# Performance work log

Hardware: AMD Instinct MI355X
Metric: run time of the kernel (lower is better)

## Reference

```python
import jax, jax.numpy as jnp
import numpy as np

N = 100000   # nodes
E = 1600000  # edges
IN = 128
H = 64
OUT = 10
NG = 128     # number of graphs
EPS = 1e-5


def _lin(k, o, i):
    kw, kb = jax.random.split(k)
    bound = 1.0 / np.sqrt(i)
    W = jax.random.uniform(kw, (o, i), jnp.float32, -bound, bound)
    b = jax.random.uniform(kb, (o,), jnp.float32, -bound, bound)
    return W, b


def setup_inputs() -> dict:
    key = jax.random.key(0)
    ks = jax.random.split(key, 10)
    x = jax.random.normal(ks[0], (N, IN), jnp.float32)
    edge_index = jax.random.randint(ks[1], (2, E), 0, N, dtype=jnp.int64)
    batch = jnp.sort(jax.random.randint(ks[2], (N,), 0, NG, dtype=jnp.int64))
    W1, b1 = _lin(ks[3], H, IN)
    W2, b2 = _lin(ks[4], H, H)
    W3, b3 = _lin(ks[5], H, H)
    Wc1, bc1 = _lin(ks[6], H, H)
    Wc2, bc2 = _lin(ks[7], OUT, H)
    ones = jnp.ones((H,), jnp.float32)
    zeros = jnp.zeros((H,), jnp.float32)
    return {
        "x": x, "edge_index": edge_index, "batch": batch,
        "W1": W1, "b1": b1, "g1": ones, "be1": zeros,
        "W2": W2, "b2": b2, "g2": ones, "be2": zeros,
        "W3": W3, "b3": b3, "g3": ones, "be3": zeros,
        "Wc1": Wc1, "bc1": bc1, "Wc2": Wc2, "bc2": bc2,
    }


def reference(x, edge_index, batch,
              W1, b1, g1, be1, W2, b2, g2, be2, W3, b3, g3, be3,
              Wc1, bc1, Wc2, bc2):
    n = x.shape[0]
    src, dst = edge_index[0], edge_index[1]
    loop = jnp.arange(n, dtype=src.dtype)
    src_a = jnp.concatenate([src, loop])  # [E+N] with self loops
    dst_a = jnp.concatenate([dst, loop])
    # degree via scatter-add (self loops included -> deg >= 1)
    deg = jax.ops.segment_sum(jnp.ones_like(dst_a, jnp.float32), dst_a, num_segments=n)
    norm = (deg[src_a] * deg[dst_a]) ** -0.5
    norm = jnp.where(jnp.isinf(norm), 0.0, norm)  # guard deg==0 (faithful to source)

    def conv(h, W, b):
        h = h @ W.T + b                       # [N, H]
        msg = h[src_a] * norm[:, None]        # gather + scale  [E+N, H]
        return jax.ops.segment_sum(msg, dst_a, num_segments=n)  # scatter-add

    def bn_relu(h, g, be):
        mu = h.mean(0)
        var = h.var(0)  # biased variance (torch BN training mode)
        return jax.nn.relu(g * (h - mu) / jnp.sqrt(var + EPS) + be)

    for (W, b, g, be) in [(W1, b1, g1, be1), (W2, b2, g2, be2), (W3, b3, g3, be3)]:
        x = bn_relu(conv(x, W, b), g, be)

    pool = jax.ops.segment_sum(x, batch, num_segments=NG)  # readout='sum'
    h = jax.nn.relu(pool @ Wc1.T + bc1)
    return h @ Wc2.T + bc2
```

## Files before the change

### kernel.cpp

```cpp
#include <hip/hip_runtime.h>
#include <hip/hip_bf16.h>


#define NN 100000
#define NE 1600000
#define INF_ 128
#define HF 64
#define OUTF 10
#define NG 128
#define NBUCK 196
#define NBLKP 512
#define CPB (NE / NBLKP)
#define NPART 32

typedef short bf16x8 __attribute__((ext_vector_type(8)));
typedef float f32x4 __attribute__((ext_vector_type(4)));

static __device__ __forceinline__ unsigned short f2bf(float x) {
    unsigned int b = __float_as_uint(x);
    b += 0x7FFFu + ((b >> 16) & 1u);
    return (unsigned short)(b >> 16);
}
static __device__ __forceinline__ float bf2f(unsigned short u) {
    return __uint_as_float(((unsigned int)u) << 16);
}
static __device__ __forceinline__ float bflo(unsigned int u) {
    return __uint_as_float(u << 16);
}
static __device__ __forceinline__ float bfhi(unsigned int u) {
    return __uint_as_float(u & 0xffff0000u);
}

__global__ __launch_bounds__(256) void kA_count(const int* __restrict__ dst,
                                                int* __restrict__ gcount) {
    __shared__ int cnt[256];
    int t = threadIdx.x, blk = blockIdx.x;
    cnt[t] = 0;
    __syncthreads();
    int beg = blk * CPB, end = beg + CPB;
    for (int i = beg + t; i < end; i += 256) atomicAdd(&cnt[dst[i] >> 9], 1);
    __syncthreads();
    if (t < NBUCK) gcount[t * NBLKP + blk] = cnt[t];
}

__global__ void k_scan1(const int* __restrict__ cnt, int* __restrict__ ro,
                        int* __restrict__ bsum, int n) {
    __shared__ int ts[256];
    int base = blockIdx.x * 1024 + threadIdx.x * 4;
    int v[4], s = 0;
#pragma unroll
    for (int k = 0; k < 4; ++k) {
        int idx = base + k;
        v[k] = (idx < n) ? cnt[idx] : 0;
        s += v[k];
    }
    ts[threadIdx.x] = s;
    __syncthreads();
    for (int off = 1; off < 256; off <<= 1) {
        int t = (threadIdx.x >= off) ? ts[threadIdx.x - off] : 0;
        __syncthreads();
        ts[threadIdx.x] += t;
        __syncthreads();
    }
    int ex = ts[threadIdx.x] - s;
    if (threadIdx.x == 255) bsum[blockIdx.x] = ts[255];
#pragma unroll
    for (int k = 0; k < 4; ++k) {
        int idx = base + k;
        if (idx < n) ro[idx] = ex;
        ex += v[k];
    }
}

__global__ void k_scan2(int* __restrict__ bsum, int nb) {
    __shared__ int ts[128];
    int i = threadIdx.x;
    int v = (i < nb) ? bsum[i] : 0;
    ts[i] = v;
    __syncthreads();
    for (int off = 1; off < 128; off <<= 1) {
        int t = (i >= off) ? ts[i - off] : 0;
        __syncthreads();
        ts[i] += t;
        __syncthreads();
    }
    if (i < nb) bsum[i] = ts[i] - v;
}

__global__ void k_scan3g(int* __restrict__ goff, const int* __restrict__ bsum, int n) {
    int i = blockIdx.x * 256 + threadIdx.x;
    if (i < n) goff[i] += bsum[i >> 10];
}

__global__ __launch_bounds__(256) void kB_part(const int* __restrict__ src,
                                               const int* __restrict__ dst,
                                               const int* __restrict__ goff,
                                               int* __restrict__ tmp) {
    __shared__ int cur[NBUCK];
    int t = threadIdx.x, blk = blockIdx.x;
    if (t < NBUCK) cur[t] = goff[t * NBLKP + blk];
    __syncthreads();
    int beg = blk * CPB, end = beg + CPB;
    for (int i = beg + t; i < end; i += 256) {
        int d = dst[i];
        int pos = atomicAdd(&cur[d >> 9], 1);
        tmp[pos] = ((d & 511) << 17) | src[i];
    }
}

__global__ __launch_bounds__(256) void kC_build(const int* __restrict__ goff,
                                                int* __restrict__ tmp,
                                                int* __restrict__ ss,
                                                int* __restrict__ ro,
                                                float* __restrict__ rdeg, int E) {
    __shared__ int cnt[512];
    __shared__ int ts[256];
    __shared__ int cur[512];
    int t = threadIdx.x, b = blockIdx.x;
    int beg = goff[b * NBLKP];
    int end = (b + 1 < NBUCK) ? goff[(b + 1) * NBLKP] : E;
    cnt[t] = 0;
    cnt[t + 256] = 0;
    __syncthreads();
    for (int i = beg + t; i < end; i += 256) atomicAdd(&cnt[tmp[i] >> 17], 1);
    __syncthreads();
    int a0 = cnt[2 * t], a1 = cnt[2 * t + 1], s = a0 + a1;
    ts[t] = s;
    __syncthreads();
    for (int off = 1; off < 256; off <<= 1) {
        int v = (t >= off) ? ts[t - off] : 0;
        __syncthreads();
        ts[t] += v;
        __syncthreads();
    }
    int ex = ts[t] - s;
    int p0 = beg + ex, p1 = beg + ex + a0;
    cur[2 * t] = p0;
    cur[2 * t + 1] = p1;
    int node0 = (b << 9) + 2 * t;
    if (node0 < NN) { ro[node0] = p0; rdeg[node0] = rsqrtf((float)a0 + 1.f); }
    else if (node0 == NN) ro[NN] = p0;
    int node1 = node0 + 1;
    if (node1 < NN) { ro[node1] = p1; rdeg[node1] = rsqrtf((float)a1 + 1.f); }
    else if (node1 == NN) ro[NN] = p1;
    __syncthreads();
    for (int i = beg + t; i < end; i += 256) {
        int p = tmp[i];
        int pos = atomicAdd(&cur[p >> 17], 1);
        ss[pos] = p & 0x1FFFF;
    }
}

__global__ void k_wpack_all(const float* __restrict__ W1f, const float* __restrict__ W2f,
                            const float* __restrict__ W3f,
                            unsigned short* __restrict__ wp0,
                            unsigned short* __restrict__ wp1,
                            unsigned short* __restrict__ wp2) {
    int b = blockIdx.x;
    const float* W;
    unsigned short* P;
    int K, base;
    if (b < 4)      { W = W1f; P = wp0; K = INF_; base = b; }
    else if (b < 6) { W = W2f; P = wp1; K = HF;   base = b - 4; }
    else            { W = W3f; P = wp2; K = HF;   base = b - 6; }
    int q = base * 256 + threadIdx.x;
    int nchunk = (K >> 5) << 8;
    if (q >= nchunk) return;
    int kb = q >> 8;
    int gq = (q >> 6) & 3;
    int ch = q & 63;
    const float* wr = W + (size_t)ch * K;
    unsigned int u[4];
#pragma unroll
    for (int i = 0; i < 4; ++i) {
        int e0 = 2 * i, e1 = 2 * i + 1;
        int k0 = kb * 32 + 4 * gq + (e0 & 3) + 16 * (e0 >> 2);
        int k1 = kb * 32 + 4 * gq + (e1 & 3) + 16 * (e1 >> 2);
        u[i] = (unsigned int)f2bf(wr[k0]) | ((unsigned int)f2bf(wr[k1]) << 16);
    }
    *(uint4*)(P + (size_t)q * 8) = make_uint4(u[0], u[1], u[2], u[3]);
}

template<int K, bool BN>
__global__ __launch_bounds__(256) void k_gemm_mfma(const float* __restrict__ Xf,
                                                   const unsigned short* __restrict__ Xh,
                                                   const unsigned short* __restrict__ Wp,
                                                   const float* __restrict__ bias,
                                                   const float* __restrict__ rdeg,
                                                   const float* __restrict__ SP,
                                                   const float* __restrict__ g,
                                                   const float* __restrict__ be,
                                                   unsigned short* __restrict__ Hs, int n) {
    constexpr int KB = K / 32;
    constexpr int RB = K * 2;
    __shared__ __align__(16) char raw[64 * 68 * 4];
    __shared__ float sa_l[64], sb_l[64];
    const int t = threadIdx.x;
    const int w = t >> 6;
    const int c = t & 15;
    const int gq = (t >> 4) & 3;
    const int r0 = blockIdx.x * 64;

    if (BN && t < 64) {
        float s = 0.f, q = 0.f;
#pragma unroll
        for (int p = 0; p < NPART; ++p) {
            s += SP[p * 128 + t];
            q += SP[p * 128 + 64 + t];
        }
        float n_ = (float)NN;
        float mu = s / n_;
        float var = q / n_ - mu * mu;
        float a = g[t] * rsqrtf(var + 1e-5f);
        sa_l[t] = a;
        sb_l[t] = be[t] - mu * a;
    }
    __syncthreads();

    {
        int r = t >> 2, q = t & 3;
        int row = r0 + r;
        int x_swz = (r & 7) << 4;
        if (BN) {
            int ch0 = q * 16;
            uint4 u0 = make_uint4(0, 0, 0, 0), u1 = make_uint4(0, 0, 0, 0);
            if (row < n) {
                const uint4* p = (const uint4*)(Xh + (size_t)row * 64 + ch0);
                u0 = p[0];
                u1 = p[1];
            }
            unsigned int uin[8] = {u0.x, u0.y, u0.z, u0.w, u1.x, u1.y, u1.z, u1.w};
            unsigned int uo[8];
#pragma unroll
            for (int j = 0; j < 8; ++j) {
                int chl = ch0 + 2 * j, chh = chl + 1;
                float v0 = fmaxf(fmaf(sa_l[chl], bflo(uin[j]), sb_l[chl]), 0.f);
                float v1 = fmaxf(fmaf(sa_l[chh], bfhi(uin[j]), sb_l[chh]), 0.f);
                uo[j] = (unsigned int)f2bf(v0) | ((unsigned int)f2bf(v1) << 16);
            }
            int b0 = r * RB + q * 32;
            *(uint4*)(raw + ((b0) ^ x_swz)) = make_uint4(uo[0], uo[1], uo[2], uo[3]);
            *(uint4*)(raw + ((b0 + 16) ^ x_swz)) = make_uint4(uo[4], uo[5], uo[6], uo[7]);
        } else {
            int ch0 = q * 32;
#pragma unroll
            for (int j2 = 0; j2 < 4; ++j2) {
                float4 a = make_float4(0.f, 0.f, 0.f, 0.f), b = make_float4(0.f, 0.f, 0.f, 0.f);
                if (row < n) {
                    const float4* p = (const float4*)(Xf + (size_t)row * K + ch0 + j2 * 8);
                    a = p[0];
                    b = p[1];
                }
                unsigned int q0 = (unsigned int)f2bf(a.x) | ((unsigned int)f2bf(a.y) << 16);
                unsigned int q1 = (unsigned int)f2bf(a.z) | ((unsigned int)f2bf(a.w) << 16);
                unsigned int q2 = (unsigned int)f2bf(b.x) | ((unsigned int)f2bf(b.y) << 16);
                unsigned int q3 = (unsigned int)f2bf(b.z) | ((unsigned int)f2bf(b.w) << 16);
                int b0 = r * RB + ch0 * 2 + j2 * 16;
                *(uint4*)(raw + (b0 ^ x_swz)) = make_uint4(q0, q1, q2, q3);
            }
        }
    }
    __syncthreads();

    bf16x8 af[KB];
    {
        int r = 16 * w + c;
        int rb = r * RB;
        int swz = (r & 7) << 4;
#pragma unroll
        for (int kb = 0; kb < KB; ++kb) {
            int off = rb + kb * 64 + gq * 8;
            uint2 u0 = *(const uint2*)(raw + (off ^ swz));
            uint2 u1 = *(const uint2*)(raw + ((off + 32) ^ swz));
            union { uint4 u; bf16x8 v; } cv;
            cv.u = make_uint4(u0.x, u0.y, u1.x, u1.y);
            af[kb] = cv.v;
        }
    }
    const uint4* wq = (const uint4*)Wp;
    f32x4 acc[4];
#pragma unroll
    for (int nn_ = 0; nn_ < 4; ++nn_) {
        acc[nn_] = (f32x4){0.f, 0.f, 0.f, 0.f};
#pragma unroll
        for (int kb = 0; kb < KB; ++kb) {
            union { uint4 u; bf16x8 v; } cw;
            cw.u = wq[(kb * 4 + gq) * 64 + nn_ * 16 + c];
            acc[nn_] = __builtin_amdgcn_mfma_f32_16x16x32_bf16(af[kb], cw.v, acc[nn_], 0, 0, 0);
        }
    }

    __syncthreads();
    float* outb = (float*)raw;
    float rv[4];
#pragma unroll
    for (int i = 0; i < 4; ++i) {
        int rg = r0 + 16 * w + 4 * gq + i;
        rv[i] = (rg < n) ? rdeg[rg] : 0.f;
    }
#pragma unroll
    for (int nn_ = 0; nn_ < 4; ++nn_) {
        int col = 16 * nn_ + c;
        float bz = bias[col];
#pragma unroll
        for (int i = 0; i < 4; ++i)
            outb[(16 * w + 4 * gq + i) * 68 + col] = (acc[nn_][i] + bz) * rv[i];
    }
    __syncthreads();
    {
        int r = t >> 2, q = t & 3;
        int row = r0 + r;
        if (row < n) {
            const float* src = outb + r * 68 + q * 16;
            unsigned int u[8];
#pragma unroll
            for (int j = 0; j < 8; ++j)
                u[j] = (unsigned int)f2bf(src[2 * j]) | ((unsigned int)f2bf(src[2 * j + 1]) << 16);
            uint4* p = (uint4*)(Hs + (size_t)row * HF + q * 16);
            p[0] = make_uint4(u[0], u[1], u[2], u[3]);
            p[1] = make_uint4(u[4], u[5], u[6], u[7]);
        }
    }
}

__global__ __launch_bounds__(256) void k_agg(const int* __restrict__ ro,
                                             const int* __restrict__ ss,
                                             const unsigned short* __restrict__ Hs,
                                             const float* __restrict__ rdeg,
                                             unsigned short* __restrict__ V16,
                                             float* __restrict__ partial, int n) {
    __shared__ float red[4][128];
    int t = threadIdx.x;
    int wid = blockIdx.x * 4 + (t >> 6);
    int lane = t & 63;
    int sub = lane >> 4;
    int lq = lane & 15;
    int c4 = lq * 4;
    int node = wid * 4 + sub;
    bool vn = node < n;
    int safe = vn ? node : 0;
    int beg = 0, d = 0;
    if (vn) {
        beg = ro[node];
        d = ro[node + 1] - beg;
    }
    float4 acc = make_float4(0.f, 0.f, 0.f, 0.f);
    if (vn) {
        uint2 u = *(const uint2*)(Hs + ((size_t)node << 6) + c4);
        acc.x = bflo(u.x); acc.y = bfhi(u.x); acc.z = bflo(u.y); acc.w = bfhi(u.y);
    }
    int dm = d;
    dm = max(dm, __shfl_xor(dm, 16));
    dm = max(dm, __shfl_xor(dm, 32));
    for (int it = 0; it < dm; it += 16) {
        int myidx = (it + lq < d) ? ss[beg + it + lq] : -1;
        int sidx[16];
        float msk[16];
#pragma unroll
        for (int k = 0; k < 16; ++k) {
            int s = __shfl(myidx, (sub << 4) + k);
            sidx[k] = (s >= 0) ? s : safe;
            msk[k] = (s >= 0) ? 1.f : 0.f;
        }
        uint2 u[16];
#pragma unroll
        for (int k = 0; k < 16; ++k)
            u[k] = *(const uint2*)(Hs + ((size_t)sidx[k] << 6) + c4);
#pragma unroll
        for (int k = 0; k < 16; ++k) {
            acc.x = fmaf(msk[k], bflo(u[k].x), acc.x);
            acc.y = fmaf(msk[k], bfhi(u[k].x), acc.y);
            acc.z = fmaf(msk[k], bflo(u[k].y), acc.z);
            acc.w = fmaf(msk[k], bfhi(u[k].y), acc.w);
        }
    }
    float rv = vn ? rdeg[node] : 0.f;
    float v0 = acc.x * rv, v1 = acc.y * rv, v2 = acc.z * rv, v3 = acc.w * rv;
    if (vn) {
        unsigned int p0 = (unsigned int)f2bf(v0) | ((unsigned int)f2bf(v1) << 16);
        unsigned int p1 = (unsigned int)f2bf(v2) | ((unsigned int)f2bf(v3) << 16);
        *(uint2*)(V16 + ((size_t)node << 6) + c4) = make_uint2(p0, p1);
    }
    float s0 = v0, s1 = v1, s2 = v2, s3 = v3;
    float q0 = v0 * v0, q1 = v1 * v1, q2 = v2 * v2, q3 = v3 * v3;
#pragma unroll
    for (int m = 16; m <= 32; m <<= 1) {
        s0 += __shfl_xor(s0, m); s1 += __shfl_xor(s1, m);
        s2 += __shfl_xor(s2, m); s3 += __shfl_xor(s3, m);
        q0 += __shfl_xor(q0, m); q1 += __shfl_xor(q1, m);
        q2 += __shfl_xor(q2, m); q3 += __shfl_xor(q3, m);
    }
    if (sub == 0) {
        int w = t >> 6;
        red[w][c4 + 0] = s0; red[w][c4 + 1] = s1;
        red[w][c4 + 2] = s2; red[w][c4 + 3] = s3;
        red[w][64 + c4 + 0] = q0; red[w][64 + c4 + 1] = q1;
        red[w][64 + c4 + 2] = q2; red[w][64 + c4 + 3] = q3;
    }
    __syncthreads();
    if (t < 128) {
        float r = red[0][t] + red[1][t] + red[2][t] + red[3][t];
        atomicAdd(&partial[(blockIdx.x & (NPART - 1)) * 128 + t], r);
    }
}

__global__ __launch_bounds__(256) void k_pool2(const unsigned short* __restrict__ V16,
                                               const float* __restrict__ SP,
                                               const float* __restrict__ g,
                                               const float* __restrict__ be,
                                               const int* __restrict__ batch,
                                               float* __restrict__ pool, int n) {
    __shared__ float sa_l[64], sb_l[64];
    int t = threadIdx.x;
    if (t < 64) {
        float s = 0.f, q = 0.f;
#pragma unroll
        for (int p = 0; p < NPART; ++p) {
            s += SP[p * 128 + t];
            q += SP[p * 128 + 64 + t];
        }
        float n_ = (float)NN;
        float mu = s / n_;
        float var = q / n_ - mu * mu;
        float a = g[t] * rsqrtf(var + 1e-5f);
        sa_l[t] = a;
        sb_l[t] = be[t] - mu * a;
    }
    __syncthreads();
    int wid = blockIdx.x * 4 + (t >> 6);
    int r0 = wid * 64;
    if (r0 >= n) return;
    int lane = t & 63;
    float sa = sa_l[lane], sb = sb_l[lane];
    int rend = min(r0 + 64, n);
    int cur = batch[r0];
    float s = 0.f;
    for (int r = r0; r < rend; ++r) {
        int b = batch[r];
        if (b != cur) {
            atomicAdd(&pool[(size_t)cur * HF + lane], s);
            s = 0.f;
            cur = b;
        }
        float v = bf2f(V16[(size_t)r * HF + lane]);
        s += fmaxf(fmaf(sa, v, sb), 0.f);
    }
    atomicAdd(&pool[(size_t)cur * HF + lane], s);
}

__global__ void k_cls(const float* __restrict__ pool, const float* __restrict__ Wc1,
                      const float* __restrict__ bc1, const float* __restrict__ Wc2,
                      const float* __restrict__ bc2, float* __restrict__ out) {
    __shared__ float pl[HF], hr[HF];
    int g = blockIdx.x, c = threadIdx.x;
    pl[c] = pool[g * HF + c];
    __syncthreads();
    float h = bc1[c];
#pragma unroll
    for (int k = 0; k < HF; ++k) h = fmaf(pl[k], Wc1[c * HF + k], h);
    hr[c] = fmaxf(h, 0.f);
    __syncthreads();
    if (c < OUTF) {
        float o = bc2[c];
#pragma unroll
        for (int k = 0; k < HF; ++k) o = fmaf(hr[k], Wc2[c * HF + k], o);
        out[g * OUTF + c] = o;
    }
}

extern "C" void kernel_launch(void* const* d_in, const int* in_sizes, int n_in,
                              void* d_out, int out_size, void* d_ws, size_t ws_size,
                              hipStream_t stream) {
    const float* x = (const float*)d_in[0];
    const int* edge = (const int*)d_in[1];
    const int* batch = (const int*)d_in[2];
    const float* W1 = (const float*)d_in[3];
    const float* b1 = (const float*)d_in[4];
    const float* g1 = (const float*)d_in[5];
    const float* be1 = (const float*)d_in[6];
    const float* W2 = (const float*)d_in[7];
    const float* b2 = (const float*)d_in[8];
    const float* g2 = (const float*)d_in[9];
    const float* be2 = (const float*)d_in[10];
    const float* W3 = (const float*)d_in[11];
    const float* b3 = (const float*)d_in[12];
    const float* g3 = (const float*)d_in[13];
    const float* be3 = (const float*)d_in[14];
    const float* Wc1 = (const float*)d_in[15];
    const float* bc1 = (const float*)d_in[16];
    const float* Wc2 = (const float*)d_in[17];
    const float* bc2 = (const float*)d_in[18];
    float* out = (float*)d_out;

    const int* src = edge;
    const int* dst = edge + NE;

    const size_t N64 = (size_t)NN * HF;
    const int NGC = NBUCK * NBLKP;
    unsigned short* V16 = (unsigned short*)d_ws;
    unsigned short* Hs = V16 + N64;
    float* rdeg = (float*)(Hs + N64);
    float* part = rdeg + NN;
    float* pool = part + 3 * NPART * 128;
    int* gcount = (int*)(pool + (size_t)NG * HF);
    int* goff = gcount + NGC;
    int* bsum = goff + NGC;
    int* ro = bsum + 128;
    int* tmp = ro + NN + 1;
    int* ss = tmp + NE;
    unsigned short* wp0 = (unsigned short*)(ss + NE);
    unsigned short* wp1 = wp0 + 8192;
    unsigned short* wp2 = wp1 + 4096;

    k_wpack_all<<<8, 256, 0, stream>>>(W1, W2, W3, wp0, wp1, wp2);

    kA_count<<<NBLKP, 256, 0, stream>>>(dst, gcount);
    const int nblk = (NGC + 1023) / 1024;
    k_scan1<<<nblk, 256, 0, stream>>>(gcount, goff, bsum, NGC);
    k_scan2<<<1, 128, 0, stream>>>(bsum, nblk);
    k_scan3g<<<(NGC + 255) / 256, 256, 0, stream>>>(goff, bsum, NGC);
    kB_part<<<NBLKP, 256, 0, stream>>>(src, dst, goff, tmp);
    kC_build<<<NBUCK, 256, 0, stream>>>(goff, tmp, ss, ro, rdeg, NE);

    hipMemsetAsync(part, 0, (3 * NPART * 128 + (size_t)NG * HF) * sizeof(float), stream);

    const unsigned short* gWp[3] = {wp0, wp1, wp2};
    const float* gb[3] = {b1, b2, b3};
    const float* gg[3] = {g1, g2, g3};
    const float* gbe[3] = {be1, be2, be3};

    const int tileblk = (NN + 63) / 64;
    const int aggblk = (NN + 15) / 16;
    const int poolblk = ((NN + 63) / 64 + 3) / 4;

    for (int l = 0; l < 3; ++l) {
        if (l == 0)
            k_gemm_mfma<INF_, false><<<tileblk, 256, 0, stream>>>(x, (const unsigned short*)0,
                                                                  gWp[0], gb[0], rdeg, part,
                                                                  gg[0], gbe[0], Hs, NN);
        else
            k_gemm_mfma<HF, true><<<tileblk, 256, 0, stream>>>((const float*)0, V16,
                                                               gWp[l], gb[l], rdeg,
                                                               part + (l - 1) * NPART * 128,
                                                               gg[l - 1], gbe[l - 1], Hs, NN);
        k_agg<<<aggblk, 256, 0, stream>>>(ro, ss, Hs, rdeg, V16,
                                          part + l * NPART * 128, NN);
        if (l == 2)
            k_pool2<<<poolblk, 256, 0, stream>>>(V16, part + 2 * NPART * 128,
                                                 gg[2], gbe[2], batch, pool, NN);
    }

    k_cls<<<NG, HF, 0, stream>>>(pool, Wc1, bc1, Wc2, bc2, out);
}
```

Measured before the change: 238.0 us.

## Merge front-end kernels, fold scan fixup into consumers, use 256-node buckets

Fuses the degree-count, weight packing and accumulator zeroing into one launch, replacing a separate pack kernel and a memset. Removes the third scan pass by having the partition and build kernels add the block prefix themselves. Halves bucket size to 256 nodes (391 buckets) so kC_build does one node per thread with more blocks in flight, at the cost of a larger count matrix to scan.

New measurement: 226.6 us, median of 2. 1.05x faster.

```diff
diff --git a/kernel.cpp b/kernel.cpp
--- a/kernel.cpp
+++ b/kernel.cpp
@@ -8,10 +8,11 @@
 #define HF 64
 #define OUTF 10
 #define NG 128
-#define NBUCK 196
+#define NBUCK 391
 #define NBLKP 512
 #define CPB (NE / NBLKP)
 #define NPART 32
+#define PARTF (3 * NPART * 128 + NG * HF)
 
 typedef short bf16x8 __attribute__((ext_vector_type(8)));
 typedef float f32x4 __attribute__((ext_vector_type(4)));
@@ -31,16 +32,52 @@
     return __uint_as_float(u & 0xffff0000u);
 }
 
-__global__ __launch_bounds__(256) void kA_count(const int* __restrict__ dst,
-                                                int* __restrict__ gcount) {
-    __shared__ int cnt[256];
-    int t = threadIdx.x, blk = blockIdx.x;
-    cnt[t] = 0;
-    __syncthreads();
-    int beg = blk * CPB, end = beg + CPB;
-    for (int i = beg + t; i < end; i += 256) atomicAdd(&cnt[dst[i] >> 9], 1);
-    __syncthreads();
-    if (t < NBUCK) gcount[t * NBLKP + blk] = cnt[t];
+__global__ __launch_bounds__(256) void k_front(const int* __restrict__ dst,
+                                               int* __restrict__ gcount,
+                                               const float* __restrict__ W1f,
+                                               const float* __restrict__ W2f,
+                                               const float* __restrict__ W3f,
+                                               unsigned short* __restrict__ wp0,
+                                               unsigned short* __restrict__ wp1,
+                                               unsigned short* __restrict__ wp2,
+                                               float* __restrict__ part) {
+    int t = threadIdx.x, b = blockIdx.x;
+    if (b < NBLKP) {
+        __shared__ int cnt[NBUCK];
+        for (int i = t; i < NBUCK; i += 256) cnt[i] = 0;
+        __syncthreads();
+        int beg = b * CPB, end = beg + CPB;
+        for (int i = beg + t; i < end; i += 256) atomicAdd(&cnt[dst[i] >> 8], 1);
+        __syncthreads();
+        for (int i = t; i < NBUCK; i += 256) gcount[i * NBLKP + b] = cnt[i];
+    } else if (b < NBLKP + 8) {
+        int bb = b - NBLKP;
+        const float* W;
+        unsigned short* P;
+        int K, base;
+        if (bb < 4)      { W = W1f; P = wp0; K = INF_; base = bb; }
+        else if (bb < 6) { W = W2f; P = wp1; K = HF;   base = bb - 4; }
+        else             { W = W3f; P = wp2; K = HF;   base = bb - 6; }
+        int q = base * 256 + t;
+        int nchunk = (K >> 5) << 8;
+        if (q >= nchunk) return;
+        int kb = q >> 8;
+        int gq = (q >> 6) & 3;
+        int ch = q & 63;
+        const float* wr = W + (size_t)ch * K;
+        unsigned int u[4];
+#pragma unroll
+        for (int i = 0; i < 4; ++i) {
+            int e0 = 2 * i, e1 = 2 * i + 1;
+            int k0 = kb * 32 + 4 * gq + (e0 & 3) + 16 * (e0 >> 2);
+            int k1 = kb * 32 + 4 * gq + (e1 & 3) + 16 * (e1 >> 2);
+            u[i] = (unsigned int)f2bf(wr[k0]) | ((unsigned int)f2bf(wr[k1]) << 16);
+        }
+        *(uint4*)(P + (size_t)q * 8) = make_uint4(u[0], u[1], u[2], u[3]);
+    } else {
+        int i = (b - NBLKP - 8) * 256 + t;
+        if (i < PARTF) part[i] = 0.f;
+    }
 }
 
 __global__ void k_scan1(const int* __restrict__ cnt, int* __restrict__ ro,
@@ -73,58 +110,62 @@
 }
 
 __global__ void k_scan2(int* __restrict__ bsum, int nb) {
-    __shared__ int ts[128];
+    __shared__ int ts[256];
     int i = threadIdx.x;
     int v = (i < nb) ? bsum[i] : 0;
     ts[i] = v;
     __syncthreads();
-    for (int off = 1; off < 128; off <<= 1) {
+    for (int off = 1; off < 256; off <<= 1) {
         int t = (i >= off) ? ts[i - off] : 0;
         __syncthreads();
         ts[i] += t;
         __syncthreads();
     }
     if (i < nb) bsum[i] = ts[i] - v;
-}
-
-__global__ void k_scan3g(int* __restrict__ goff, const int* __restrict__ bsum, int n) {
-    int i = blockIdx.x * 256 + threadIdx.x;
-    if (i < n) goff[i] += bsum[i >> 10];
 }
 
 __global__ __launch_bounds__(256) void kB_part(const int* __restrict__ src,
                                                const int* __restrict__ dst,
                                                const int* __restrict__ goff,
+                                               const int* __restrict__ bsum,
                                                int* __restrict__ tmp) {
     __shared__ int cur[NBUCK];
     int t = threadIdx.x, blk = blockIdx.x;
-    if (t < NBUCK) cur[t] = goff[t * NBLKP + blk];
+    for (int i = t; i < NBUCK; i += 256) {
+        int idx = i * NBLKP + blk;
+        cur[i] = goff[idx] + bsum[idx >> 10];
+    }
     __syncthreads();
     int beg = blk * CPB, end = beg + CPB;
     for (int i = beg + t; i < end; i += 256) {
         int d = dst[i];
-        int pos = atomicAdd(&cur[d >> 9], 1);
-        tmp[pos] = ((d & 511) << 17) | src[i];
+        int pos = atomicAdd(&cur[d >> 8], 1);
+        tmp[pos] = ((d & 255) << 17) | src[i];
     }
 }
 
 __global__ __launch_bounds__(256) void kC_build(const int* __restrict__ goff,
+                                                const int* __restrict__ bsum,
                                                 int* __restrict__ tmp,
                                                 int* __restrict__ ss,
                                                 int* __restrict__ ro,
                                                 float* __restrict__ rdeg, int E) {
-    __shared__ int cnt[512];
+    __shared__ int cnt[256];
     __shared__ int ts[256];
-    __shared__ int cur[512];
+    __shared__ int cur[256];
     int t = threadIdx.x, b = blockIdx.x;
-    int beg = goff[b * NBLKP];
-    int end = (b + 1 < NBUCK) ? goff[(b + 1) * NBLKP] : E;
+    int i0 = b * NBLKP;
+    int beg = goff[i0] + bsum[i0 >> 10];
+    int end = E;
+    if (b + 1 < NBUCK) {
+        int i1 = (b + 1) * NBLKP;
+        end = goff[i1] + bsum[i1 >> 10];
+    }
     cnt[t] = 0;
-    cnt[t + 256] = 0;
     __syncthreads();
     for (int i = beg + t; i < end; i += 256) atomicAdd(&cnt[tmp[i] >> 17], 1);
     __syncthreads();
-    int a0 = cnt[2 * t], a1 = cnt[2 * t + 1], s = a0 + a1;
+    int s = cnt[t];
     ts[t] = s;
     __syncthreads();
     for (int off = 1; off < 256; off <<= 1) {
@@ -133,52 +174,21 @@
         ts[t] += v;
         __syncthreads();
     }
-    int ex = ts[t] - s;
-    int p0 = beg + ex, p1 = beg + ex + a0;
-    cur[2 * t] = p0;
-    cur[2 * t + 1] = p1;
-    int node0 = (b << 9) + 2 * t;
-    if (node0 < NN) { ro[node0] = p0; rdeg[node0] = rsqrtf((float)a0 + 1.f); }
-    else if (node0 == NN) ro[NN] = p0;
-    int node1 = node0 + 1;
-    if (node1 < NN) { ro[node1] = p1; rdeg[node1] = rsqrtf((float)a1 + 1.f); }
-    else if (node1 == NN) ro[NN] = p1;
+    int p = beg + ts[t] - s;
+    cur[t] = p;
+    int node = (b << 8) + t;
+    if (node < NN) {
+        ro[node] = p;
+        rdeg[node] = rsqrtf((float)s + 1.f);
+    } else if (node == NN) {
+        ro[NN] = p;
+    }
     __syncthreads();
     for (int i = beg + t; i < end; i += 256) {
-        int p = tmp[i];
-        int pos = atomicAdd(&cur[p >> 17], 1);
-        ss[pos] = p & 0x1FFFF;
-    }
-}
-
-__global__ void k_wpack_all(const float* __restrict__ W1f, const float* __restrict__ W2f,
-                            const float* __restrict__ W3f,
-                            unsigned short* __restrict__ wp0,
-                            unsigned short* __restrict__ wp1,
-                            unsigned short* __restrict__ wp2) {
-    int b = blockIdx.x;
-    const float* W;
-    unsigned short* P;
-    int K, base;
-    if (b < 4)      { W = W1f; P = wp0; K = INF_; base = b; }
-    else if (b < 6) { W = W2f; P = wp1; K = HF;   base = b - 4; }
-    else            { W = W3f; P = wp2; K = HF;   base = b - 6; }
-    int q = base * 256 + threadIdx.x;
-    int nchunk = (K >> 5) << 8;
-    if (q >= nchunk) return;
-    int kb = q >> 8;
-    int gq = (q >> 6) & 3;
-    int ch = q & 63;
-    const float* wr = W + (size_t)ch * K;
-    unsigned int u[4];
-#pragma unroll
-    for (int i = 0; i < 4; ++i) {
-        int e0 = 2 * i, e1 = 2 * i + 1;
-        int k0 = kb * 32 + 4 * gq + (e0 & 3) + 16 * (e0 >> 2);
-        int k1 = kb * 32 + 4 * gq + (e1 & 3) + 16 * (e1 >> 2);
-        u[i] = (unsigned int)f2bf(wr[k0]) | ((unsigned int)f2bf(wr[k1]) << 16);
-    }
-    *(uint4*)(P + (size_t)q * 8) = make_uint4(u[0], u[1], u[2], u[3]);
+        int pk = tmp[i];
+        int pos = atomicAdd(&cur[pk >> 17], 1);
+        ss[pos] = pk & 0x1FFFF;
+    }
 }
 
 template<int K, bool BN>
@@ -505,24 +515,21 @@
     int* gcount = (int*)(pool + (size_t)NG * HF);
     int* goff = gcount + NGC;
     int* bsum = goff + NGC;
-    int* ro = bsum + 128;
+    int* ro = bsum + 256;
     int* tmp = ro + NN + 1;
     int* ss = tmp + NE;
     unsigned short* wp0 = (unsigned short*)(ss + NE);
     unsigned short* wp1 = wp0 + 8192;
     unsigned short* wp2 = wp1 + 4096;
 
-    k_wpack_all<<<8, 256, 0, stream>>>(W1, W2, W3, wp0, wp1, wp2);
-
-    kA_count<<<NBLKP, 256, 0, stream>>>(dst, gcount);
+    k_front<<<NBLKP + 8 + (PARTF + 255) / 256, 256, 0, stream>>>(
+        dst, gcount, W1, W2, W3, wp0, wp1, wp2, part);
+
     const int nblk = (NGC + 1023) / 1024;
     k_scan1<<<nblk, 256, 0, stream>>>(gcount, goff, bsum, NGC);
-    k_scan2<<<1, 128, 0, stream>>>(bsum, nblk);
-    k_scan3g<<<(NGC + 255) / 256, 256, 0, stream>>>(goff, bsum, NGC);
-    kB_part<<<NBLKP, 256, 0, stream>>>(src, dst, goff, tmp);
-    kC_build<<<NBUCK, 256, 0, stream>>>(goff, tmp, ss, ro, rdeg, NE);
-
-    hipMemsetAsync(part, 0, (3 * NPART * 128 + (size_t)NG * HF) * sizeof(float), stream);
+    k_scan2<<<1, 256, 0, stream>>>(bsum, nblk);
+    kB_part<<<NBLKP, 256, 0, stream>>>(src, dst, goff, bsum, tmp);
+    kC_build<<<NBUCK, 256, 0, stream>>>(goff, bsum, tmp, ss, ro, rdeg, NE);
 
     const unsigned short* gWp[3] = {wp0, wp1, wp2};
     const float* gb[3] = {b1, b2, b3};
```
